# Performance work log

Measured on AMD Instinct MI355X. Metric: run time of the kernel, lower is better.

## Reference

```python
import jax, jax.numpy as jnp
import numpy as np

N = 10000        # nodes
E = 640000       # edges (before self-loops)
IN = 128         # in_channels
HID = 32         # hidden_channels
HEADS = 4
HC = HID * HEADS # 128
OUT = 40         # out_channels
NEG_SLOPE = 0.2  # PyG GATConv default


def setup_inputs() -> dict:
    key = jax.random.key(0)
    ks = jax.random.split(key, 12)
    g = lambda k, shape: (jax.random.normal(k, shape, jnp.float32) * 0.1)
    return {
        "x": jax.random.normal(ks[0], (N, IN), jnp.float32),
        "edge_index": jax.random.randint(ks[1], (2, E), 0, N, dtype=jnp.int32),
        # conv1: in -> HID per head, HEADS heads, concat
        "W1": g(ks[2], (IN, HEADS * HID)),
        "a_src1": g(ks[3], (HEADS, HID)),
        "a_dst1": g(ks[4], (HEADS, HID)),
        "b1": jnp.zeros((HEADS * HID,), jnp.float32),
        # conv2: HC -> HC, 1 head
        "W2": g(ks[5], (HC, HC)),
        "a_src2": g(ks[6], (1, HC)),
        "a_dst2": g(ks[7], (1, HC)),
        "b2": jnp.zeros((HC,), jnp.float32),
        # final linear head
        "Wlin": g(ks[8], (HC, OUT)),
        "blin": jnp.zeros((OUT,), jnp.float32),
    }


def _gat_layer(x, W, a_src, a_dst, b, src, dst, heads, n):
    """PyG-style GATConv: gather -> edge attention -> segment softmax -> scatter."""
    d = W.shape[1] // heads
    h = (x @ W).reshape(n, heads, d)                       # [N, H, d]
    asrc = jnp.einsum('nhd,hd->nh', h, a_src)              # [N, H]
    adst = jnp.einsum('nhd,hd->nh', h, a_dst)
    e = jax.nn.leaky_relu(asrc[src] + adst[dst], NEG_SLOPE)  # [E, H]
    m = jax.ops.segment_max(e, dst, num_segments=n)          # per-dst max (stable softmax)
    p = jnp.exp(e - m[dst])
    z = jax.ops.segment_sum(p, dst, num_segments=n)
    alpha = p / (z[dst] + 1e-16)                             # [E, H]
    out = jax.ops.segment_sum(h[src] * alpha[:, :, None], dst, num_segments=n)
    return out.reshape(n, heads * d) + b


def reference(x, edge_index, W1, a_src1, a_dst1, b1, W2, a_src2, a_dst2, b2, Wlin, blin):
    n = x.shape[0]
    loop = jnp.arange(n, dtype=edge_index.dtype)           # add_self_loops=True
    src = jnp.concatenate([edge_index[0], loop])
    dst = jnp.concatenate([edge_index[1], loop])
    # eval mode: dropout is identity
    h1 = jax.nn.elu(_gat_layer(x, W1, a_src1, a_dst1, b1, src, dst, HEADS, n))
    h2 = jax.nn.elu(_gat_layer(h1, W2, a_src2, a_dst2, b2, src, dst, 1, n))
    return h2 @ Wlin + blin
```

## Files before the change

kernel.cpp:

```cpp
#include <hip/hip_runtime.h>
#include <hip/hip_bf16.h>

#define KSUB 8
#define SUBCAP 32
#define CAP 256

__global__ void fused_csr_gemm4(const int* __restrict__ srcArr, const int* __restrict__ dstArr,
                                int E, int N, int* __restrict__ deg2, int* __restrict__ csr,
                                const float* __restrict__ x, const float* __restrict__ W,
                                const float* __restrict__ a_src, const float* __restrict__ a_dst,
                                __hip_bfloat16* __restrict__ hwb, float* __restrict__ asrc,
                                float* __restrict__ adst, int NC, int NG) {
    __shared__ float xr[8][128];
    int tid = threadIdx.x;
    int pair = blockIdx.x >> 1;
    if ((blockIdx.x & 1) == 0) {
        if (pair >= NC) return;
        int k_sub = pair & (KSUB - 1);
        int Etot = E + N;
        int base = pair * 512 + tid;
#pragma unroll
        for (int k = 0; k < 4; k++) {
            int i = base + k * 128;
            if (i < Etot) {
                int s, d;
                if (i < E) { s = srcArr[i]; d = dstArr[i]; }
                else       { s = d = i - E; }
                int p = atomicAdd(&deg2[d * KSUB + k_sub], 1);
                if (p < SUBCAP) csr[d * CAP + k_sub * SUBCAP + p] = s;
            }
        }
        return;
    }
    if (pair >= NG) return;
    const int NB = 8;
    int n0 = pair * NB;
    int j = tid;
    for (int r = 0; r < NB; r++) {
        int nn = n0 + r;
        xr[r][j] = (nn < N) ? x[nn * 128 + j] : 0.f;
    }
    __syncthreads();
    float acc[NB];
#pragma unroll
    for (int r = 0; r < NB; r++) acc[r] = 0.f;
    for (int k = 0; k < 128; k++) {
        float w = W[k * 128 + j];
#pragma unroll
        for (int r = 0; r < NB; r++) acc[r] += xr[r][k] * w;
    }
    int h = j >> 5;
    float as = a_src[j];
    float ad = a_dst[j];
    for (int r = 0; r < NB; r++) {
        int nn = n0 + r;
        if (nn < N) hwb[nn * 128 + j] = __float2bfloat16(acc[r]);
        float vs = acc[r] * as;
        float vd = acc[r] * ad;
        for (int off = 16; off >= 1; off >>= 1) {
            vs += __shfl_xor(vs, off);
            vd += __shfl_xor(vd, off);
        }
        if ((j & 31) == 0 && nn < N) { asrc[nn * 4 + h] = vs; adst[nn * 4 + h] = vd; }
    }
}

__global__ void gemm_att1(const float* __restrict__ x, const float* __restrict__ W,
                          const float* __restrict__ a_src, const float* __restrict__ a_dst,
                          __hip_bfloat16* __restrict__ hwb, float* __restrict__ asrc,
                          float* __restrict__ adst, int N) {
    const int NB = 8;
    int n0 = blockIdx.x * NB;
    int j = threadIdx.x;
    __shared__ float xr[NB][128];
    __shared__ float tmp[4];
    for (int r = 0; r < NB; r++) {
        int nn = n0 + r;
        xr[r][j] = (nn < N) ? x[nn * 128 + j] : 0.f;
    }
    __syncthreads();
    float acc[NB];
#pragma unroll
    for (int r = 0; r < NB; r++) acc[r] = 0.f;
    for (int k = 0; k < 128; k++) {
        float w = W[k * 128 + j];
#pragma unroll
        for (int r = 0; r < NB; r++) acc[r] += xr[r][k] * w;
    }
    float as = a_src[j];
    float ad = a_dst[j];
    for (int r = 0; r < NB; r++) {
        int nn = n0 + r;
        if (nn < N) hwb[nn * 128 + j] = __float2bfloat16(acc[r]);
        float vs = acc[r] * as;
        float vd = acc[r] * ad;
        for (int off = 32; off >= 1; off >>= 1) {
            vs += __shfl_xor(vs, off);
            vd += __shfl_xor(vd, off);
        }
        if ((j & 63) == 0) { tmp[(j >> 6) * 2] = vs; tmp[(j >> 6) * 2 + 1] = vd; }
        __syncthreads();
        if (j == 0 && nn < N) { asrc[nn] = tmp[0] + tmp[2]; adst[nn] = tmp[1] + tmp[3]; }
        __syncthreads();
    }
}

__device__ __forceinline__ int slot8(int idx, const int* pref) {
    int k = 0;
#pragma unroll
    for (int j = 1; j < KSUB; j++) k += (idx >= pref[j]);
    return k * SUBCAP + (idx - pref[k]);
}

__global__ __launch_bounds__(64) void agg4(const __hip_bfloat16* __restrict__ hw,
                     const float* __restrict__ asrc, const float* __restrict__ adst,
                     const int* __restrict__ deg2, const int* __restrict__ csr_src,
                     const float* __restrict__ b, float* __restrict__ y, int N) {
    int n = blockIdx.x;
    int t = threadIdx.x;
    const int4* dp = (const int4*)&deg2[n * KSUB];
    int4 ca = dp[0], cb = dp[1];
    int pref[KSUB];
    int cnts[KSUB] = { min(ca.x,SUBCAP), min(ca.y,SUBCAP), min(ca.z,SUBCAP), min(ca.w,SUBCAP),
                       min(cb.x,SUBCAP), min(cb.y,SUBCAP), min(cb.z,SUBCAP), min(cb.w,SUBCAP) };
    pref[0] = 0;
#pragma unroll
    for (int k = 1; k < KSUB; k++) pref[k] = pref[k-1] + cnts[k-1];
    int deg = pref[KSUB-1] + cnts[KSUB-1];
    const unsigned* hwu = (const unsigned*)hw;
    __shared__ float pe[64 * 4];
    __shared__ int se[64];
    float4 adl = *(const float4*)&adst[n * 4];
    int hcol = t >> 4;
    float2 acc = make_float2(0.f, 0.f);
    float z0 = 0.f, z1 = 0.f, z2 = 0.f, z3 = 0.f;
    for (int base = 0; base < deg; base += 64) {
        int cnt = min(64, deg - base);
        __syncthreads();
        if (t < cnt) {
            int s = csr_src[n * CAP + slot8(base + t, pref)];
            se[t] = s;
            float4 av = *(const float4*)&asrc[s * 4];
            float e0 = av.x + adl.x, e1 = av.y + adl.y;
            float e2 = av.z + adl.z, e3 = av.w + adl.w;
            e0 = e0 > 0.f ? e0 : 0.2f * e0;
            e1 = e1 > 0.f ? e1 : 0.2f * e1;
            e2 = e2 > 0.f ? e2 : 0.2f * e2;
            e3 = e3 > 0.f ? e3 : 0.2f * e3;
            float p0 = __expf(e0), p1 = __expf(e1), p2 = __expf(e2), p3 = __expf(e3);
            pe[t * 4 + 0] = p0; pe[t * 4 + 1] = p1;
            pe[t * 4 + 2] = p2; pe[t * 4 + 3] = p3;
            z0 += p0; z1 += p1; z2 += p2; z3 += p3;
        }
        __syncthreads();
        for (int c = 0; c < cnt; c++) {
            int s = se[c];
            float p = pe[c * 4 + hcol];
            unsigned v = hwu[s * 64 + t];
            acc.x += p * __uint_as_float(v << 16);
            acc.y += p * __uint_as_float(v & 0xffff0000u);
        }
    }
    for (int off = 32; off >= 1; off >>= 1) {
        z0 += __shfl_xor(z0, off); z1 += __shfl_xor(z1, off);
        z2 += __shfl_xor(z2, off); z3 += __shfl_xor(z3, off);
    }
    float z = (hcol == 0) ? z0 : (hcol == 1) ? z1 : (hcol == 2) ? z2 : z3;
    float inv = 1.f / (z + 1e-16f);
    float2 bb = *(const float2*)&b[t * 2];
    float r0 = acc.x * inv + bb.x;
    float r1 = acc.y * inv + bb.y;
    r0 = r0 > 0.f ? r0 : (__expf(r0) - 1.0f);
    r1 = r1 > 0.f ? r1 : (__expf(r1) - 1.0f);
    *(float2*)&y[n * 128 + t * 2] = make_float2(r0, r1);
}

__global__ __launch_bounds__(64) void agg1_lin(const __hip_bfloat16* __restrict__ hw,
                         const float* __restrict__ asrc, const float* __restrict__ adst,
                         const int* __restrict__ deg2, const int* __restrict__ csr_src,
                         const float* __restrict__ b, const float* __restrict__ Wl,
                         const float* __restrict__ bl, float* __restrict__ out,
                         int N, int OUTC) {
    int n = blockIdx.x;
    int t = threadIdx.x;
    const int4* dp = (const int4*)&deg2[n * KSUB];
    int4 ca = dp[0], cb = dp[1];
    int pref[KSUB];
    int cnts[KSUB] = { min(ca.x,SUBCAP), min(ca.y,SUBCAP), min(ca.z,SUBCAP), min(ca.w,SUBCAP),
                       min(cb.x,SUBCAP), min(cb.y,SUBCAP), min(cb.z,SUBCAP), min(cb.w,SUBCAP) };
    pref[0] = 0;
#pragma unroll
    for (int k = 1; k < KSUB; k++) pref[k] = pref[k-1] + cnts[k-1];
    int deg = pref[KSUB-1] + cnts[KSUB-1];
    const unsigned* hwu = (const unsigned*)hw;
    __shared__ float pe[64];
    __shared__ int se[64];
    __shared__ float yrow[128];
    float adl = adst[n];
    float2 acc = make_float2(0.f, 0.f);
    float zp = 0.f;
    for (int base = 0; base < deg; base += 64) {
        int cnt = min(64, deg - base);
        __syncthreads();
        if (t < cnt) {
            int s = csr_src[n * CAP + slot8(base + t, pref)];
            se[t] = s;
            float e = asrc[s] + adl;
            e = e > 0.f ? e : 0.2f * e;
            float p = __expf(e);
            pe[t] = p;
            zp += p;
        }
        __syncthreads();
        for (int c = 0; c < cnt; c++) {
            int s = se[c];
            float p = pe[c];
            unsigned v = hwu[s * 64 + t];
            acc.x += p * __uint_as_float(v << 16);
            acc.y += p * __uint_as_float(v & 0xffff0000u);
        }
    }
    for (int off = 32; off >= 1; off >>= 1) zp += __shfl_xor(zp, off);
    float inv = 1.f / (zp + 1e-16f);
    float2 bb = *(const float2*)&b[t * 2];
    float r0 = acc.x * inv + bb.x;
    float r1 = acc.y * inv + bb.y;
    r0 = r0 > 0.f ? r0 : (__expf(r0) - 1.0f);
    r1 = r1 > 0.f ? r1 : (__expf(r1) - 1.0f);
    yrow[t * 2] = r0; yrow[t * 2 + 1] = r1;
    __syncthreads();
    if (t < OUTC) {
        float a = bl[t];
        for (int k = 0; k < 128; k++) a += yrow[k] * Wl[k * OUTC + t];
        out[n * OUTC + t] = a;
    }
}

extern "C" void kernel_launch(void* const* d_in, const int* in_sizes, int n_in,
                              void* d_out, int out_size, void* d_ws, size_t ws_size,
                              hipStream_t stream) {
    const float* x       = (const float*)d_in[0];
    const int*   ei      = (const int*)d_in[1];
    const float* W1      = (const float*)d_in[2];
    const float* a_src1  = (const float*)d_in[3];
    const float* a_dst1  = (const float*)d_in[4];
    const float* b1      = (const float*)d_in[5];
    const float* W2      = (const float*)d_in[6];
    const float* a_src2  = (const float*)d_in[7];
    const float* a_dst2  = (const float*)d_in[8];
    const float* b2      = (const float*)d_in[9];
    const float* Wlin    = (const float*)d_in[10];
    const float* blin    = (const float*)d_in[11];
    float* out = (float*)d_out;

    const int N = in_sizes[0] / 128;
    const int E = in_sizes[1] / 2;
    const int OUTC = in_sizes[10] / 128;
    const int Etot = E + N;
    const int* src = ei;
    const int* dst = ei + E;
    const int NG = (N + 7) / 8;
    const int NC = (Etot + 511) / 512;
    const int NMAX = (NC > NG) ? NC : NG;

    char* w = (char*)d_ws;
    size_t off = 0;
    auto alloc = [&](size_t bytes) -> char* {
        char* p = w + off;
        off += (bytes + 255) & ~(size_t)255;
        return p;
    };
    int*             deg2  = (int*)alloc((size_t)N * KSUB * 4);
    int*             csr   = (int*)alloc((size_t)N * CAP * 4);
    __hip_bfloat16*  hwb   = (__hip_bfloat16*)alloc((size_t)N * 128 * 2);
    float*           bufY  = (float*)alloc((size_t)N * 128 * 4);
    float*           asrc1 = (float*)alloc((size_t)N * 4 * 4);
    float*           adst1 = (float*)alloc((size_t)N * 4 * 4);
    float*           asrc2 = (float*)alloc((size_t)N * 4);
    float*           adst2 = (float*)alloc((size_t)N * 4);
    (void)ws_size;

    hipMemsetAsync(deg2, 0, (size_t)N * KSUB * 4, stream);
    fused_csr_gemm4<<<2 * NMAX, 128, 0, stream>>>(src, dst, E, N, deg2, csr,
                                                  x, W1, a_src1, a_dst1, hwb, asrc1, adst1,
                                                  NC, NG);

    agg4<<<N, 64, 0, stream>>>(hwb, asrc1, adst1, deg2, csr, b1, bufY, N);

    gemm_att1<<<NG, 128, 0, stream>>>(bufY, W2, a_src2, a_dst2, hwb, asrc2, adst2, N);
    agg1_lin<<<N, 64, 0, stream>>>(hwb, asrc2, adst2, deg2, csr, b2, Wlin, blin, out, N, OUTC);
}
```

Before: 174.6 us.

## Store CSR source indices as 16-bit and pack two nodes per aggregation block

The CSR neighbour list now stores source indices as unsigned short instead of int, halving CSR write and read traffic. This is valid only while N is below 65536, which holds for the current N of 10000. The aggregation kernels now run two nodes per 128-thread block, one wavefront each, with per-wave shared buffers, halving the number of blocks launched. Because the block-wide barriers are shared, each wave loops over the larger of the two degrees, so one wave can sit idle while the other finishes.

```diff
diff --git a/kernel.cpp b/kernel.cpp
--- a/kernel.cpp
+++ b/kernel.cpp
@@ -6,7 +6,8 @@
 #define CAP 256
 
 __global__ void fused_csr_gemm4(const int* __restrict__ srcArr, const int* __restrict__ dstArr,
-                                int E, int N, int* __restrict__ deg2, int* __restrict__ csr,
+                                int E, int N, int* __restrict__ deg2,
+                                unsigned short* __restrict__ csr,
                                 const float* __restrict__ x, const float* __restrict__ W,
                                 const float* __restrict__ a_src, const float* __restrict__ a_dst,
                                 __hip_bfloat16* __restrict__ hwb, float* __restrict__ asrc,
@@ -27,7 +28,7 @@
                 if (i < E) { s = srcArr[i]; d = dstArr[i]; }
                 else       { s = d = i - E; }
                 int p = atomicAdd(&deg2[d * KSUB + k_sub], 1);
-                if (p < SUBCAP) csr[d * CAP + k_sub * SUBCAP + p] = s;
+                if (p < SUBCAP) csr[d * CAP + k_sub * SUBCAP + p] = (unsigned short)s;
             }
         }
         return;
@@ -112,34 +113,48 @@
     return k * SUBCAP + (idx - pref[k]);
 }
 
-__global__ __launch_bounds__(64) void agg4(const __hip_bfloat16* __restrict__ hw,
+__global__ __launch_bounds__(128) void agg4(const __hip_bfloat16* __restrict__ hw,
                      const float* __restrict__ asrc, const float* __restrict__ adst,
-                     const int* __restrict__ deg2, const int* __restrict__ csr_src,
+                     const int* __restrict__ deg2, const unsigned short* __restrict__ csr_src,
                      const float* __restrict__ b, float* __restrict__ y, int N) {
-    int n = blockIdx.x;
-    int t = threadIdx.x;
-    const int4* dp = (const int4*)&deg2[n * KSUB];
-    int4 ca = dp[0], cb = dp[1];
+    int t  = threadIdx.x & 63;
+    int wv = threadIdx.x >> 6;
+    int n  = blockIdx.x * 2 + wv;
+    bool active = (n < N);
     int pref[KSUB];
-    int cnts[KSUB] = { min(ca.x,SUBCAP), min(ca.y,SUBCAP), min(ca.z,SUBCAP), min(ca.w,SUBCAP),
-                       min(cb.x,SUBCAP), min(cb.y,SUBCAP), min(cb.z,SUBCAP), min(cb.w,SUBCAP) };
-    pref[0] = 0;
-#pragma unroll
-    for (int k = 1; k < KSUB; k++) pref[k] = pref[k-1] + cnts[k-1];
-    int deg = pref[KSUB-1] + cnts[KSUB-1];
+    int deg = 0;
+    if (active) {
+        const int4* dp = (const int4*)&deg2[n * KSUB];
+        int4 ca = dp[0], cb = dp[1];
+        int cnts[KSUB] = { min(ca.x,SUBCAP), min(ca.y,SUBCAP), min(ca.z,SUBCAP), min(ca.w,SUBCAP),
+                           min(cb.x,SUBCAP), min(cb.y,SUBCAP), min(cb.z,SUBCAP), min(cb.w,SUBCAP) };
+        pref[0] = 0;
+#pragma unroll
+        for (int k = 1; k < KSUB; k++) pref[k] = pref[k-1] + cnts[k-1];
+        deg = pref[KSUB-1] + cnts[KSUB-1];
+    } else {
+#pragma unroll
+        for (int k = 0; k < KSUB; k++) pref[k] = 0;
+    }
+    __shared__ int degs[2];
+    __shared__ float pe[2][64 * 4];
+    __shared__ int se[2][64];
+    if (t == 0) degs[wv] = deg;
+    __syncthreads();
+    int chunks = (max(degs[0], degs[1]) + 63) >> 6;
     const unsigned* hwu = (const unsigned*)hw;
-    __shared__ float pe[64 * 4];
-    __shared__ int se[64];
-    float4 adl = *(const float4*)&adst[n * 4];
+    float4 adl = active ? *(const float4*)&adst[n * 4] : make_float4(0.f,0.f,0.f,0.f);
     int hcol = t >> 4;
     float2 acc = make_float2(0.f, 0.f);
     float z0 = 0.f, z1 = 0.f, z2 = 0.f, z3 = 0.f;
-    for (int base = 0; base < deg; base += 64) {
-        int cnt = min(64, deg - base);
-        __syncthreads();
-        if (t < cnt) {
-            int s = csr_src[n * CAP + slot8(base + t, pref)];
-            se[t] = s;
+    for (int ch = 0; ch < chunks; ch++) {
+        int base = ch * 64;
+        int cnt = deg - base;
+        if (cnt > 64) cnt = 64;
+        __syncthreads();
+        if (active && t < cnt) {
+            int s = (int)csr_src[n * CAP + slot8(base + t, pref)];
+            se[wv][t] = s;
             float4 av = *(const float4*)&asrc[s * 4];
             float e0 = av.x + adl.x, e1 = av.y + adl.y;
             float e2 = av.z + adl.z, e3 = av.w + adl.w;
@@ -148,14 +163,14 @@
             e2 = e2 > 0.f ? e2 : 0.2f * e2;
             e3 = e3 > 0.f ? e3 : 0.2f * e3;
             float p0 = __expf(e0), p1 = __expf(e1), p2 = __expf(e2), p3 = __expf(e3);
-            pe[t * 4 + 0] = p0; pe[t * 4 + 1] = p1;
-            pe[t * 4 + 2] = p2; pe[t * 4 + 3] = p3;
+            pe[wv][t * 4 + 0] = p0; pe[wv][t * 4 + 1] = p1;
+            pe[wv][t * 4 + 2] = p2; pe[wv][t * 4 + 3] = p3;
             z0 += p0; z1 += p1; z2 += p2; z3 += p3;
         }
         __syncthreads();
         for (int c = 0; c < cnt; c++) {
-            int s = se[c];
-            float p = pe[c * 4 + hcol];
+            int s = se[wv][c];
+            float p = pe[wv][c * 4 + hcol];
             unsigned v = hwu[s * 64 + t];
             acc.x += p * __uint_as_float(v << 16);
             acc.y += p * __uint_as_float(v & 0xffff0000u);
@@ -165,6 +180,7 @@
         z0 += __shfl_xor(z0, off); z1 += __shfl_xor(z1, off);
         z2 += __shfl_xor(z2, off); z3 += __shfl_xor(z3, off);
     }
+    if (!active) return;
     float z = (hcol == 0) ? z0 : (hcol == 1) ? z1 : (hcol == 2) ? z2 : z3;
     float inv = 1.f / (z + 1e-16f);
     float2 bb = *(const float2*)&b[t * 2];
@@ -175,46 +191,60 @@
     *(float2*)&y[n * 128 + t * 2] = make_float2(r0, r1);
 }
 
-__global__ __launch_bounds__(64) void agg1_lin(const __hip_bfloat16* __restrict__ hw,
+__global__ __launch_bounds__(128) void agg1_lin(const __hip_bfloat16* __restrict__ hw,
                          const float* __restrict__ asrc, const float* __restrict__ adst,
-                         const int* __restrict__ deg2, const int* __restrict__ csr_src,
+                         const int* __restrict__ deg2, const unsigned short* __restrict__ csr_src,
                          const float* __restrict__ b, const float* __restrict__ Wl,
                          const float* __restrict__ bl, float* __restrict__ out,
                          int N, int OUTC) {
-    int n = blockIdx.x;
-    int t = threadIdx.x;
-    const int4* dp = (const int4*)&deg2[n * KSUB];
-    int4 ca = dp[0], cb = dp[1];
+    int t  = threadIdx.x & 63;
+    int wv = threadIdx.x >> 6;
+    int n  = blockIdx.x * 2 + wv;
+    bool active = (n < N);
     int pref[KSUB];
-    int cnts[KSUB] = { min(ca.x,SUBCAP), min(ca.y,SUBCAP), min(ca.z,SUBCAP), min(ca.w,SUBCAP),
-                       min(cb.x,SUBCAP), min(cb.y,SUBCAP), min(cb.z,SUBCAP), min(cb.w,SUBCAP) };
-    pref[0] = 0;
-#pragma unroll
-    for (int k = 1; k < KSUB; k++) pref[k] = pref[k-1] + cnts[k-1];
-    int deg = pref[KSUB-1] + cnts[KSUB-1];
+    int deg = 0;
+    if (active) {
+        const int4* dp = (const int4*)&deg2[n * KSUB];
+        int4 ca = dp[0], cb = dp[1];
+        int cnts[KSUB] = { min(ca.x,SUBCAP), min(ca.y,SUBCAP), min(ca.z,SUBCAP), min(ca.w,SUBCAP),
+                           min(cb.x,SUBCAP), min(cb.y,SUBCAP), min(cb.z,SUBCAP), min(cb.w,SUBCAP) };
+        pref[0] = 0;
+#pragma unroll
+        for (int k = 1; k < KSUB; k++) pref[k] = pref[k-1] + cnts[k-1];
+        deg = pref[KSUB-1] + cnts[KSUB-1];
+    } else {
+#pragma unroll
+        for (int k = 0; k < KSUB; k++) pref[k] = 0;
+    }
+    __shared__ int degs[2];
+    __shared__ float pe[2][64];
+    __shared__ int se[2][64];
+    __shared__ float yrow[2][128];
+    if (t == 0) degs[wv] = deg;
+    __syncthreads();
+    int chunks = (max(degs[0], degs[1]) + 63) >> 6;
     const unsigned* hwu = (const unsigned*)hw;
-    __shared__ float pe[64];
-    __shared__ int se[64];
-    __shared__ float yrow[128];
-    float adl = adst[n];
+    float adl = active ? adst[n] : 0.f;
     float2 acc = make_float2(0.f, 0.f);
     float zp = 0.f;
-    for (int base = 0; base < deg; base += 64) {
-        int cnt = min(64, deg - base);
-        __syncthreads();
-        if (t < cnt) {
-            int s = csr_src[n * CAP + slot8(base + t, pref)];
-            se[t] = s;
+    for (int ch = 0; ch < chunks; ch++) {
+        int base = ch * 64;
+        int cnt = deg - base;
+        if (cnt > 64) cnt = 64;
+        __syncthreads();
+        if (active && t < cnt) {
+            int s = (int)csr_src[n * CAP + slot8(base + t, pref)];
+            se[wv][t] = s;
             float e = asrc[s] + adl;
             e = e > 0.f ? e : 0.2f * e;
             float p = __expf(e);
-            pe[t] = p;
+            pe[wv][t] = p;
             zp += p;
         }
         __syncthreads();
         for (int c = 0; c < cnt; c++) {
-            int s = se[c];
-            float p = pe[c];
+            int s = se[wv][c];
+            float p = pe[wv][c];
             unsigned v = hwu[s * 64 + t];
             acc.x += p * __uint_as_float(v << 16);
             acc.y += p * __uint_as_float(v & 0xffff0000u);
@@ -227,11 +257,11 @@
     float r1 = acc.y * inv + bb.y;
     r0 = r0 > 0.f ? r0 : (__expf(r0) - 1.0f);
     r1 = r1 > 0.f ? r1 : (__expf(r1) - 1.0f);
-    yrow[t * 2] = r0; yrow[t * 2 + 1] = r1;
-    __syncthreads();
-    if (t < OUTC) {
+    yrow[wv][t * 2] = r0; yrow[wv][t * 2 + 1] = r1;
+    __syncthreads();
+    if (active && t < OUTC) {
         float a = bl[t];
-        for (int k = 0; k < 128; k++) a += yrow[k] * Wl[k * OUTC + t];
+        for (int k = 0; k < 128; k++) a += yrow[wv][k] * Wl[k * OUTC + t];
         out[n * OUTC + t] = a;
     }
 }
@@ -271,7 +301,7 @@
         return p;
     };
     int*             deg2  = (int*)alloc((size_t)N * KSUB * 4);
-    int*             csr   = (int*)alloc((size_t)N * CAP * 4);
+    unsigned short*  csr   = (unsigned short*)alloc((size_t)N * CAP * 2);
     __hip_bfloat16*  hwb   = (__hip_bfloat16*)alloc((size_t)N * 128 * 2);
     float*           bufY  = (float*)alloc((size_t)N * 128 * 4);
     float*           asrc1 = (float*)alloc((size_t)N * 4 * 4);
@@ -285,8 +315,9 @@
                                                   x, W1, a_src1, a_dst1, hwb, asrc1, adst1,
                                                   NC, NG);
 
-    agg4<<<N, 64, 0, stream>>>(hwb, asrc1, adst1, deg2, csr, b1, bufY, N);
+    agg4<<<(N + 1) / 2, 128, 0, stream>>>(hwb, asrc1, adst1, deg2, csr, b1, bufY, N);
 
     gemm_att1<<<NG, 128, 0, stream>>>(bufY, W2, a_src2, a_dst2, hwb, asrc2, adst2, N);
-    agg1_lin<<<N, 64, 0, stream>>>(hwb, asrc2, adst2, deg2, csr, b2, Wlin, blin, out, N, OUTC);
-}
+    agg1_lin<<<(N + 1) / 2, 128, 0, stream>>>(hwb, asrc2, adst2, deg2, csr, b2, Wlin, blin,
+                                              out, N, OUTC);
+}
```

Result: no change. 175.6 us (+0.6%).

## Use bf16 MFMA for both GAT projections, unfuse CSR build, use 16-bit CSR indices

Applied to the files above, without the earlier changes.

Replaces the scalar fp32 GEMM kernels for both layers with a wave-level bf16 MFMA GEMM (16x16x32), using weights pre-transposed and converted to bf16 by a small prep kernel. The attention logits are computed from the MFMA accumulators. CSR construction moves into its own kernel with larger blocks and now stores source indices as unsigned short, halving CSR memory traffic. Both inputs and weights are rounded to bf16 before the matmul, which lowers precision. The 16-bit indices only hold for N below 65536, and the GEMM has no tail guard for N not divisible by 16.

```diff
diff --git a/kernel.cpp b/kernel.cpp
--- a/kernel.cpp
+++ b/kernel.cpp
@@ -5,103 +5,129 @@
 #define SUBCAP 32
 #define CAP 256
 
-__global__ void fused_csr_gemm4(const int* __restrict__ srcArr, const int* __restrict__ dstArr,
-                                int E, int N, int* __restrict__ deg2, int* __restrict__ csr,
-                                const float* __restrict__ x, const float* __restrict__ W,
-                                const float* __restrict__ a_src, const float* __restrict__ a_dst,
-                                __hip_bfloat16* __restrict__ hwb, float* __restrict__ asrc,
-                                float* __restrict__ adst, int NC, int NG) {
-    __shared__ float xr[8][128];
+using bf16x8 = __attribute__((ext_vector_type(8))) short;
+using f32x4  = __attribute__((ext_vector_type(4))) float;
+
+static __device__ __forceinline__ short f2b(float f) {
+    __hip_bfloat16 h = __float2bfloat16(f);
+    return *reinterpret_cast<short*>(&h);
+}
+
+__global__ void build_csr(const int* __restrict__ srcArr, const int* __restrict__ dstArr,
+                          int E, int N, int* __restrict__ deg2,
+                          unsigned short* __restrict__ csr) {
     int tid = threadIdx.x;
-    int pair = blockIdx.x >> 1;
-    if ((blockIdx.x & 1) == 0) {
-        if (pair >= NC) return;
-        int k_sub = pair & (KSUB - 1);
-        int Etot = E + N;
-        int base = pair * 512 + tid;
-#pragma unroll
-        for (int k = 0; k < 4; k++) {
-            int i = base + k * 128;
-            if (i < Etot) {
-                int s, d;
-                if (i < E) { s = srcArr[i]; d = dstArr[i]; }
-                else       { s = d = i - E; }
-                int p = atomicAdd(&deg2[d * KSUB + k_sub], 1);
-                if (p < SUBCAP) csr[d * CAP + k_sub * SUBCAP + p] = s;
+    int k_sub = blockIdx.x & (KSUB - 1);
+    int Etot = E + N;
+    int base = blockIdx.x * 1024 + tid;
+#pragma unroll
+    for (int k = 0; k < 4; k++) {
+        int i = base + k * 256;
+        if (i < Etot) {
+            int s, d;
+            if (i < E) { s = srcArr[i]; d = dstArr[i]; }
+            else       { s = d = i - E; }
+            int p = atomicAdd(&deg2[d * KSUB + k_sub], 1);
+            if (p < SUBCAP) csr[d * CAP + k_sub * SUBCAP + p] = (unsigned short)s;
+        }
+    }
+}
+
+__global__ __launch_bounds__(256) void prep_w(const float* __restrict__ W1,
+                                              const float* __restrict__ W2,
+                                              short* __restrict__ Wt1,
+                                              short* __restrict__ Wt2) {
+    __shared__ float t[32][33];
+    int which = blockIdx.x >> 4;
+    int tile = blockIdx.x & 15;
+    int bi = tile >> 2, bj = tile & 3;
+    const float* W = which ? W2 : W1;
+    short* Wt = which ? Wt2 : Wt1;
+    int tx = threadIdx.x & 31, ty = threadIdx.x >> 5;
+#pragma unroll
+    for (int i = 0; i < 4; i++) {
+        int r = bi * 32 + ty + 8 * i;
+        t[ty + 8 * i][tx] = W[r * 128 + bj * 32 + tx];
+    }
+    __syncthreads();
+#pragma unroll
+    for (int i = 0; i < 4; i++) {
+        int j = bj * 32 + ty + 8 * i;
+        Wt[j * 128 + bi * 32 + tx] = f2b(t[tx][ty + 8 * i]);
+    }
+}
+
+template <int H>
+__global__ __launch_bounds__(256) void gemm_mfma(const float* __restrict__ x,
+                        const short* __restrict__ Wt,
+                        const float* __restrict__ a_src, const float* __restrict__ a_dst,
+                        __hip_bfloat16* __restrict__ hwb, float* __restrict__ asrc,
+                        float* __restrict__ adst, int N) {
+    int wave = (blockIdx.x * 256 + threadIdx.x) >> 6;
+    int lane = threadIdx.x & 63;
+    int n0 = wave * 16;
+    if (n0 >= N) return;
+    int m = lane & 15, q = lane >> 4;
+    int row = n0 + m;
+    bf16x8 afrag[4];
+    const float* xr = x + (size_t)row * 128 + q * 8;
+#pragma unroll
+    for (int kt = 0; kt < 4; kt++) {
+        float4 v0 = *(const float4*)(xr + kt * 32);
+        float4 v1 = *(const float4*)(xr + kt * 32 + 4);
+        bf16x8 f;
+        f[0] = f2b(v0.x); f[1] = f2b(v0.y); f[2] = f2b(v0.z); f[3] = f2b(v0.w);
+        f[4] = f2b(v1.x); f[5] = f2b(v1.y); f[6] = f2b(v1.z); f[7] = f2b(v1.w);
+        afrag[kt] = f;
+    }
+    float vs[4] = {0.f, 0.f, 0.f, 0.f}, vd[4] = {0.f, 0.f, 0.f, 0.f};
+#pragma unroll
+    for (int ct = 0; ct < 8; ct++) {
+        f32x4 acc = {0.f, 0.f, 0.f, 0.f};
+        const short* wrow = Wt + (ct * 16 + m) * 128 + q * 8;
+#pragma unroll
+        for (int kt = 0; kt < 4; kt++) {
+            bf16x8 bfrag = *(const bf16x8*)(wrow + kt * 32);
+            acc = __builtin_amdgcn_mfma_f32_16x16x32_bf16(afrag[kt], bfrag, acc, 0, 0, 0);
+        }
+        int col = ct * 16 + m;
+        float asv = a_src[col], adv = a_dst[col];
+#pragma unroll
+        for (int r = 0; r < 4; r++) {
+            int rr = n0 + q * 4 + r;
+            hwb[rr * 128 + col] = __float2bfloat16(acc[r]);
+            vs[r] += acc[r] * asv;
+            vd[r] += acc[r] * adv;
+        }
+        if (H == 4 && (ct & 1) == 1) {
+#pragma unroll
+            for (int r = 0; r < 4; r++) {
+                float a = vs[r], d = vd[r];
+                for (int off = 8; off >= 1; off >>= 1) {
+                    a += __shfl_xor(a, off); d += __shfl_xor(d, off);
+                }
+                if (m == 0) {
+                    int rr = n0 + q * 4 + r;
+                    asrc[rr * 4 + (ct >> 1)] = a;
+                    adst[rr * 4 + (ct >> 1)] = d;
+                }
+                vs[r] = 0.f; vd[r] = 0.f;
             }
         }
-        return;
-    }
-    if (pair >= NG) return;
-    const int NB = 8;
-    int n0 = pair * NB;
-    int j = tid;
-    for (int r = 0; r < NB; r++) {
-        int nn = n0 + r;
-        xr[r][j] = (nn < N) ? x[nn * 128 + j] : 0.f;
-    }
-    __syncthreads();
-    float acc[NB];
-#pragma unroll
-    for (int r = 0; r < NB; r++) acc[r] = 0.f;
-    for (int k = 0; k < 128; k++) {
-        float w = W[k * 128 + j];
-#pragma unroll
-        for (int r = 0; r < NB; r++) acc[r] += xr[r][k] * w;
-    }
-    int h = j >> 5;
-    float as = a_src[j];
-    float ad = a_dst[j];
-    for (int r = 0; r < NB; r++) {
-        int nn = n0 + r;
-        if (nn < N) hwb[nn * 128 + j] = __float2bfloat16(acc[r]);
-        float vs = acc[r] * as;
-        float vd = acc[r] * ad;
-        for (int off = 16; off >= 1; off >>= 1) {
-            vs += __shfl_xor(vs, off);
-            vd += __shfl_xor(vd, off);
-        }
-        if ((j & 31) == 0 && nn < N) { asrc[nn * 4 + h] = vs; adst[nn * 4 + h] = vd; }
-    }
-}
-
-__global__ void gemm_att1(const float* __restrict__ x, const float* __restrict__ W,
-                          const float* __restrict__ a_src, const float* __restrict__ a_dst,
-                          __hip_bfloat16* __restrict__ hwb, float* __restrict__ asrc,
-                          float* __restrict__ adst, int N) {
-    const int NB = 8;
-    int n0 = blockIdx.x * NB;
-    int j = threadIdx.x;
-    __shared__ float xr[NB][128];
-    __shared__ float tmp[4];
-    for (int r = 0; r < NB; r++) {
-        int nn = n0 + r;
-        xr[r][j] = (nn < N) ? x[nn * 128 + j] : 0.f;
-    }
-    __syncthreads();
-    float acc[NB];
-#pragma unroll
-    for (int r = 0; r < NB; r++) acc[r] = 0.f;
-    for (int k = 0; k < 128; k++) {
-        float w = W[k * 128 + j];
-#pragma unroll
-        for (int r = 0; r < NB; r++) acc[r] += xr[r][k] * w;
-    }
-    float as = a_src[j];
-    float ad = a_dst[j];
-    for (int r = 0; r < NB; r++) {
-        int nn = n0 + r;
-        if (nn < N) hwb[nn * 128 + j] = __float2bfloat16(acc[r]);
-        float vs = acc[r] * as;
-        float vd = acc[r] * ad;
-        for (int off = 32; off >= 1; off >>= 1) {
-            vs += __shfl_xor(vs, off);
-            vd += __shfl_xor(vd, off);
-        }
-        if ((j & 63) == 0) { tmp[(j >> 6) * 2] = vs; tmp[(j >> 6) * 2 + 1] = vd; }
-        __syncthreads();
-        if (j == 0 && nn < N) { asrc[nn] = tmp[0] + tmp[2]; adst[nn] = tmp[1] + tmp[3]; }
-        __syncthreads();
+    }
+    if (H == 1) {
+#pragma unroll
+        for (int r = 0; r < 4; r++) {
+            float a = vs[r], d = vd[r];
+            for (int off = 8; off >= 1; off >>= 1) {
+                a += __shfl_xor(a, off); d += __shfl_xor(d, off);
+            }
+            if (m == 0) {
+                int rr = n0 + q * 4 + r;
+                asrc[rr] = a;
+                adst[rr] = d;
+            }
+        }
     }
 }
 
@@ -114,7 +140,7 @@
 
 __global__ __launch_bounds__(64) void agg4(const __hip_bfloat16* __restrict__ hw,
                      const float* __restrict__ asrc, const float* __restrict__ adst,
-                     const int* __restrict__ deg2, const int* __restrict__ csr_src,
+                     const int* __restrict__ deg2, const unsigned short* __restrict__ csr_src,
                      const float* __restrict__ b, float* __restrict__ y, int N) {
     int n = blockIdx.x;
     int t = threadIdx.x;
@@ -138,7 +164,7 @@
         int cnt = min(64, deg - base);
         __syncthreads();
         if (t < cnt) {
-            int s = csr_src[n * CAP + slot8(base + t, pref)];
+            int s = (int)csr_src[n * CAP + slot8(base + t, pref)];
             se[t] = s;
             float4 av = *(const float4*)&asrc[s * 4];
             float e0 = av.x + adl.x, e1 = av.y + adl.y;
@@ -177,7 +203,7 @@
 
 __global__ __launch_bounds__(64) void agg1_lin(const __hip_bfloat16* __restrict__ hw,
                          const float* __restrict__ asrc, const float* __restrict__ adst,
-                         const int* __restrict__ deg2, const int* __restrict__ csr_src,
+                         const int* __restrict__ deg2, const unsigned short* __restrict__ csr_src,
                          const float* __restrict__ b, const float* __restrict__ Wl,
                          const float* __restrict__ bl, float* __restrict__ out,
                          int N, int OUTC) {
@@ -203,7 +229,7 @@
         int cnt = min(64, deg - base);
         __syncthreads();
         if (t < cnt) {
-            int s = csr_src[n * CAP + slot8(base + t, pref)];
+            int s = (int)csr_src[n * CAP + slot8(base + t, pref)];
             se[t] = s;
             float e = asrc[s] + adl;
             e = e > 0.f ? e : 0.2f * e;
@@ -259,9 +285,8 @@
     const int Etot = E + N;
     const int* src = ei;
     const int* dst = ei + E;
-    const int NG = (N + 7) / 8;
-    const int NC = (Etot + 511) / 512;
-    const int NMAX = (NC > NG) ? NC : NG;
+    const int NCB = (Etot + 1023) / 1024;
+    const int NGB = (N / 16 + 3) / 4;
 
     char* w = (char*)d_ws;
     size_t off = 0;
@@ -271,9 +296,11 @@
         return p;
     };
     int*             deg2  = (int*)alloc((size_t)N * KSUB * 4);
-    int*             csr   = (int*)alloc((size_t)N * CAP * 4);
+    unsigned short*  csr   = (unsigned short*)alloc((size_t)N * CAP * 2);
     __hip_bfloat16*  hwb   = (__hip_bfloat16*)alloc((size_t)N * 128 * 2);
     float*           bufY  = (float*)alloc((size_t)N * 128 * 4);
+    short*           Wt1   = (short*)alloc((size_t)128 * 128 * 2);
+    short*           Wt2   = (short*)alloc((size_t)128 * 128 * 2);
     float*           asrc1 = (float*)alloc((size_t)N * 4 * 4);
     float*           adst1 = (float*)alloc((size_t)N * 4 * 4);
     float*           asrc2 = (float*)alloc((size_t)N * 4);
@@ -281,12 +308,12 @@
     (void)ws_size;
 
     hipMemsetAsync(deg2, 0, (size_t)N * KSUB * 4, stream);
-    fused_csr_gemm4<<<2 * NMAX, 128, 0, stream>>>(src, dst, E, N, deg2, csr,
-                                                  x, W1, a_src1, a_dst1, hwb, asrc1, adst1,
-                                                  NC, NG);
-
+    prep_w<<<32, 256, 0, stream>>>(W1, W2, Wt1, Wt2);
+    build_csr<<<NCB, 256, 0, stream>>>(src, dst, E, N, deg2, csr);
+
+    gemm_mfma<4><<<NGB, 256, 0, stream>>>(x, Wt1, a_src1, a_dst1, hwb, asrc1, adst1, N);
     agg4<<<N, 64, 0, stream>>>(hwb, asrc1, adst1, deg2, csr, b1, bufY, N);
 
-    gemm_att1<<<NG, 128, 0, stream>>>(bufY, W2, a_src2, a_dst2, hwb, asrc2, adst2, N);
+    gemm_mfma<1><<<NGB, 256, 0, stream>>>(bufY, Wt2, a_src2, a_dst2, hwb, asrc2, adst2, N);
     agg1_lin<<<N, 64, 0, stream>>>(hwb, asrc2, adst2, deg2, csr, b2, Wlin, blin, out, N, OUTC);
 }
```

Measured after the change: 172.8 us. No clear change (-1.0%).
